# Optimization experiments

Measured on AMD Instinct MI355X. Metric: run time of the kernel, lower is better.

Reference implementation:

```python
import jax, jax.numpy as jnp
import numpy as np
from jax import lax

NBITS = 8
QMAX_SYM = 2 ** (NBITS - 1) - 1  # 127
QMIN_SYM = -(2 ** (NBITS - 1))   # -128
QMAX_ASYM = 2 ** NBITS - 1       # 255


def fake_quant_sym(x):
    # symmetric per-tensor fake quant with straight-through estimator
    delta = lax.stop_gradient(jnp.max(jnp.abs(x))) / QMAX_SYM + 1e-8
    q = jnp.clip(jnp.round(x / delta), QMIN_SYM, QMAX_SYM) * delta
    return x + lax.stop_gradient(q - x)


def fake_quant_asym(x):
    # asymmetric per-tensor fake quant (for softmax output) with STE
    xmin = lax.stop_gradient(jnp.min(x))
    xmax = lax.stop_gradient(jnp.max(x))
    delta = (xmax - xmin) / QMAX_ASYM + 1e-8
    zp = jnp.round(-xmin / delta)
    q = (jnp.clip(jnp.round(x / delta) + zp, 0, QMAX_ASYM) - zp) * delta
    return x + lax.stop_gradient(q - x)


def layer_norm(x, g, b, eps=1e-5):
    mu = jnp.mean(x, axis=-1, keepdims=True)
    var = jnp.var(x, axis=-1, keepdims=True)
    return (x - mu) * lax.rsqrt(var + eps) * g + b


def setup_inputs() -> dict:
    key = jax.random.key(0)
    ks = jax.random.split(key, 8)
    B, N, C = 8, 4096, 256
    s = 0.02
    return {
        "x": jax.random.normal(ks[0], (B, N, C), jnp.float32),
        "q_w": jax.random.normal(ks[1], (C, C), jnp.float32) * s,
        "q_b": jnp.zeros((C,), jnp.float32),
        "kv_w": jax.random.normal(ks[2], (2 * C, C), jnp.float32) * s,
        "kv_b": jnp.zeros((2 * C,), jnp.float32),
        "sr_w": jax.random.normal(ks[3], (C, C, 4, 4), jnp.float32) * s,
        "sr_b": jnp.zeros((C,), jnp.float32),
        "norm_g": jnp.ones((C,), jnp.float32),
        "norm_b": jnp.zeros((C,), jnp.float32),
        "proj_w": jax.random.normal(ks[4], (C, C), jnp.float32) * s,
        "proj_b": jnp.zeros((C,), jnp.float32),
        "H": 64,
        "W": 64,
    }


def reference(x, q_w, q_b, kv_w, kv_b, sr_w, sr_b, norm_g, norm_b, proj_w, proj_b, H, W):
    B, N, C = x.shape
    num_heads = 8
    sr_ratio = 4
    dh = C // num_heads
    scale = dh ** -0.5

    # weight fake-quant (PreQuantModule, sym=True)
    q_wq = fake_quant_sym(q_w)
    kv_wq = fake_quant_sym(kv_w)
    sr_wq = fake_quant_sym(sr_w)
    proj_wq = fake_quant_sym(proj_w)

    # q projection -> [B, heads, N, dh], post-act sym fake quant
    q = (jnp.einsum('bnc,dc->bnd', x, q_wq) + q_b)
    q = fake_quant_sym(q.reshape(B, N, num_heads, dh).transpose(0, 2, 1, 3))

    # spatial reduction: x -> [B,C,H,W], conv k=stride=sr_ratio, then LayerNorm
    x_ = x.transpose(0, 2, 1).reshape(B, C, H, W)
    x_ = lax.conv_general_dilated(x_, sr_wq, (sr_ratio, sr_ratio), 'VALID',
                                  dimension_numbers=('NCHW', 'OIHW', 'NCHW'))
    x_ = x_ + sr_b[None, :, None, None]
    N2 = (H // sr_ratio) * (W // sr_ratio)
    x_ = x_.reshape(B, C, N2).transpose(0, 2, 1)  # [B, N2, C]
    x_ = layer_norm(x_, norm_g, norm_b)

    # kv projection -> k, v [B, heads, N2, dh], post-act sym fake quant
    kv = jnp.einsum('bnc,dc->bnd', x_, kv_wq) + kv_b
    kv = kv.reshape(B, N2, 2, num_heads, dh).transpose(2, 0, 3, 1, 4)
    k = fake_quant_sym(kv[0])
    v = fake_quant_sym(kv[1])

    # attention with asym fake quant on softmax output
    attn = jnp.einsum('bhnd,bhmd->bhnm', q, k) * scale
    attn = jax.nn.softmax(attn, axis=-1)
    attn = fake_quant_asym(attn)

    out = jnp.einsum('bhnm,bhmd->bhnd', attn, v)
    out = out.transpose(0, 2, 1, 3).reshape(B, N, C)
    out = jnp.einsum('bnc,dc->bnd', out, proj_wq) + proj_b
    return out
```

## Files before the change

kernel.cpp:

```cpp
#include <hip/hip_runtime.h>
#include <stdint.h>

typedef float f32x4 __attribute__((ext_vector_type(4)));
typedef __bf16 bf16x8 __attribute__((ext_vector_type(8)));

#define DEV __device__ __forceinline__

DEV unsigned short f2bf(float f) {
  unsigned u = __float_as_uint(f);
  u += 0x7FFFu + ((u >> 16) & 1u);
  return (unsigned short)(u >> 16);
}

DEV float exp2_(float x) {
#if __has_builtin(__builtin_amdgcn_exp2f)
  return __builtin_amdgcn_exp2f(x);
#else
  return exp2f(x);
#endif
}

DEV unsigned cvtpk(float lo, float hi) {
  unsigned r;
  asm("v_cvt_pk_bf16_f32 %0, %1, %2" : "=v"(r) : "v"(lo), "v"(hi));
  return r;
}

DEV void pl32swap(unsigned &a, unsigned &b) {
#if __has_builtin(__builtin_amdgcn_permlane32_swap)
  auto r = __builtin_amdgcn_permlane32_swap(a, b, false, false);
  a = r[0]; b = r[1];
#else
  asm("v_permlane32_swap_b32 %0, %1" : "+v"(a), "+v"(b));
#endif
}

DEV void pl16swap(unsigned &a, unsigned &b) {
#if __has_builtin(__builtin_amdgcn_permlane16_swap)
  auto r = __builtin_amdgcn_permlane16_swap(a, b, false, false);
  a = r[0]; b = r[1];
#else
  asm("v_permlane16_swap_b32 %0, %1" : "+v"(a), "+v"(b));
#endif
}

__global__ void k_init(float* scal) {
  int t = threadIdx.x;
  if (t < 16) scal[t] = (t == 7) ? __uint_as_float(0x7f800000u) : 0.f;
}

__global__ __launch_bounds__(256) void k_absmax4(const float* w0, const float* w1,
                                                 const float* w2, const float* w3, float* scal) {
  const float* srcs[4] = {w0, w1, w2, w3};
  const int ns[4] = {65536, 131072, 1048576, 65536};
  int t = blockIdx.y;
  const float* src = srcs[t];
  int n = ns[t];
  float m = 0.f;
  for (int i = blockIdx.x * 256 + threadIdx.x; i < n; i += gridDim.x * 256)
    m = fmaxf(m, fabsf(src[i]));
  #pragma unroll
  for (int d = 1; d < 64; d <<= 1) m = fmaxf(m, __shfl_xor(m, d, 64));
  __shared__ float red[4];
  if ((threadIdx.x & 63) == 0) red[threadIdx.x >> 6] = m;
  __syncthreads();
  if (threadIdx.x == 0) {
    m = fmaxf(fmaxf(red[0], red[1]), fmaxf(red[2], red[3]));
    atomicMax((unsigned*)(scal + t), __float_as_uint(m));
  }
}

__global__ __launch_bounds__(256) void k_quantw(const float* qw, const float* kvw,
                                                const float* prw, const float* srw,
                                                const float* xf,
                                                unsigned short* qo, unsigned short* kvo,
                                                unsigned short* pro, unsigned short* sro,
                                                unsigned short* xbo,
                                                const float* scal) {
  int bx = blockIdx.x;
  int tid = bx * 256 + threadIdx.x;
  {
    int oo = tid >> 12;
    int rem = tid & 4095;
    int khkw = rem >> 8;
    int i = rem & 255;
    float delta = scal[2] / 127.f + 1e-8f;
    float x = srw[oo * 4096 + i * 16 + khkw];
    sro[tid] = f2bf(fminf(fmaxf(rintf(x / delta), -128.f), 127.f) * delta);
  }
  {
    const float4* xs = (const float4*)(xf + (size_t)tid * 8);
    float4 v0 = xs[0], v1 = xs[1];
    unsigned w0 = ((unsigned)f2bf(v0.y) << 16) | f2bf(v0.x);
    unsigned w1 = ((unsigned)f2bf(v0.w) << 16) | f2bf(v0.z);
    unsigned w2 = ((unsigned)f2bf(v1.y) << 16) | f2bf(v1.x);
    unsigned w3 = ((unsigned)f2bf(v1.w) << 16) | f2bf(v1.z);
    *(uint4*)(xbo + (size_t)tid * 8) = make_uint4(w0, w1, w2, w3);
  }
  if (bx < 512) {
    float delta = scal[1] / 127.f + 1e-8f;
    kvo[tid] = f2bf(fminf(fmaxf(rintf(kvw[tid] / delta), -128.f), 127.f) * delta);
  }
  if (bx < 256) {
    float dq = scal[0] / 127.f + 1e-8f;
    qo[tid] = f2bf(fminf(fmaxf(rintf(qw[tid] / dq), -128.f), 127.f) * dq);
    float dp = scal[3] / 127.f + 1e-8f;
    pro[tid] = f2bf(fminf(fmaxf(rintf(prw[tid] / dp), -128.f), 127.f) * dp);
  }
}

__global__ __launch_bounds__(256) void k_gemm_bk(const unsigned short* __restrict__ Ab,
                                                 const unsigned short* __restrict__ W,
                                                 const float* __restrict__ bias,
                                                 float* __restrict__ C,
                                                 int M, int N, float* max_ptr, int split) {
  __shared__ unsigned short As[64 * 136];
  __shared__ unsigned short Bs[64 * 136];
  const int m0 = blockIdx.y * 64, n0 = blockIdx.x * 64;
  const int tid = threadIdx.x;
  const int wid = tid >> 6, lane = tid & 63;
  const int quad = lane >> 4, lr = lane & 15;
  const int wm = wid >> 1, wn = wid & 1;
  f32x4 acc[2][2] = {};
  for (int kb = 0; kb < 256; kb += 128) {
    __syncthreads();
    #pragma unroll
    for (int i = 0; i < 4; i++) {
      int c = i * 256 + tid;
      int row = c >> 4, cu = (c & 15) * 8;
      *(uint4*)&As[row * 136 + cu] = *(const uint4*)(Ab + (size_t)(m0 + row) * 256 + kb + cu);
      *(uint4*)&Bs[row * 136 + cu] = *(const uint4*)(W + (size_t)(n0 + row) * 256 + kb + cu);
    }
    __syncthreads();
    #pragma unroll
    for (int kc = 0; kc < 4; kc++) {
      bf16x8 af0 = *(const bf16x8*)&As[(wm * 32 + lr) * 136 + kc * 32 + quad * 8];
      bf16x8 af1 = *(const bf16x8*)&As[(wm * 32 + 16 + lr) * 136 + kc * 32 + quad * 8];
      bf16x8 bf0 = *(const bf16x8*)&Bs[(wn * 32 + lr) * 136 + kc * 32 + quad * 8];
      bf16x8 bf1 = *(const bf16x8*)&Bs[(wn * 32 + 16 + lr) * 136 + kc * 32 + quad * 8];
      acc[0][0] = __builtin_amdgcn_mfma_f32_16x16x32_bf16(af0, bf0, acc[0][0], 0, 0, 0);
      acc[0][1] = __builtin_amdgcn_mfma_f32_16x16x32_bf16(af0, bf1, acc[0][1], 0, 0, 0);
      acc[1][0] = __builtin_amdgcn_mfma_f32_16x16x32_bf16(af1, bf0, acc[1][0], 0, 0, 0);
      acc[1][1] = __builtin_amdgcn_mfma_f32_16x16x32_bf16(af1, bf1, acc[1][1], 0, 0, 0);
    }
  }
  float amax = 0.f;
  #pragma unroll
  for (int mi = 0; mi < 2; mi++)
    #pragma unroll
    for (int ni = 0; ni < 2; ni++) {
      int col = n0 + wn * 32 + ni * 16 + lr;
      float bv = bias[col];
      #pragma unroll
      for (int r = 0; r < 4; r++) {
        int row = m0 + wm * 32 + mi * 16 + quad * 4 + r;
        float v = acc[mi][ni][r] + bv;
        C[(size_t)row * N + col] = v;
        amax = fmaxf(amax, fabsf(v));
      }
    }
  if (max_ptr) {
    #pragma unroll
    for (int d = 1; d < 64; d <<= 1) amax = fmaxf(amax, __shfl_xor(amax, d, 64));
    if (lane == 0) {
      int slot = (split > 0 && n0 >= split) ? 1 : 0;
      atomicMax((unsigned*)(max_ptr + slot), __float_as_uint(amax));
    }
  }
}

__global__ __launch_bounds__(256) void k_gemm128(const unsigned short* __restrict__ Ab,
                                                 const unsigned short* __restrict__ W,
                                                 const float* __restrict__ bias,
                                                 float* __restrict__ C,
                                                 float* max_ptr) {
  __shared__ unsigned short As[128 * 72];
  __shared__ unsigned short Bs[128 * 72];
  const int id = blockIdx.x;
  const int xcd = id & 7, idx = id >> 3;
  const int mt = xcd * 32 + (idx >> 1), nt = idx & 1;
  const int m0 = mt * 128, n0 = nt * 128;
  const int tid = threadIdx.x;
  const int wid = tid >> 6, lane = tid & 63;
  const int quad = lane >> 4, lr = lane & 15;
  const int wm = wid >> 1, wn = wid & 1;
  f32x4 acc[4][4] = {};
  for (int kb = 0; kb < 256; kb += 64) {
    __syncthreads();
    #pragma unroll
    for (int i = 0; i < 4; i++) {
      int c = i * 256 + tid;
      int row = c >> 3, cu = (c & 7) * 8;
      *(uint4*)&As[row * 72 + cu] = *(const uint4*)(Ab + (size_t)(m0 + row) * 256 + kb + cu);
      *(uint4*)&Bs[row * 72 + cu] = *(const uint4*)(W + (size_t)(n0 + row) * 256 + kb + cu);
    }
    __syncthreads();
    #pragma unroll
    for (int kc = 0; kc < 2; kc++) {
      bf16x8 af[4], bf[4];
      #pragma unroll
      for (int mi = 0; mi < 4; mi++)
        af[mi] = *(const bf16x8*)&As[(wm * 64 + mi * 16 + lr) * 72 + kc * 32 + quad * 8];
      #pragma unroll
      for (int ni = 0; ni < 4; ni++)
        bf[ni] = *(const bf16x8*)&Bs[(wn * 64 + ni * 16 + lr) * 72 + kc * 32 + quad * 8];
      #pragma unroll
      for (int mi = 0; mi < 4; mi++)
        #pragma unroll
        for (int ni = 0; ni < 4; ni++)
          acc[mi][ni] = __builtin_amdgcn_mfma_f32_16x16x32_bf16(af[mi], bf[ni], acc[mi][ni], 0, 0, 0);
    }
  }
  float amax = 0.f;
  #pragma unroll
  for (int mi = 0; mi < 4; mi++)
    #pragma unroll
    for (int ni = 0; ni < 4; ni++) {
      int col = n0 + wn * 64 + ni * 16 + lr;
      float bv = bias[col];
      #pragma unroll
      for (int r = 0; r < 4; r++) {
        int row = m0 + wm * 64 + mi * 16 + quad * 4 + r;
        float v = acc[mi][ni][r] + bv;
        C[(size_t)row * 256 + col] = v;
        amax = fmaxf(amax, fabsf(v));
      }
    }
  if (max_ptr) {
    #pragma unroll
    for (int d = 1; d < 64; d <<= 1) amax = fmaxf(amax, __shfl_xor(amax, d, 64));
    if (lane == 0) atomicMax((unsigned*)max_ptr, __float_as_uint(amax));
  }
}

__global__ __launch_bounds__(256) void k_conv_sk(const unsigned short* __restrict__ xb,
                                                 const unsigned short* __restrict__ W,
                                                 float* __restrict__ C) {
  __shared__ unsigned short As[64 * 136];
  __shared__ unsigned short Bs[64 * 136];
  const int id = blockIdx.x;
  const int xcd = id & 7, idx = id >> 3;
  const int a = idx >> 2, nt = idx & 3;
  const int ag = xcd * 16 + a;
  const int mt = ag & 31, z = ag >> 5;
  const int m0 = mt * 64, n0 = nt * 64;
  const int kOff = z * 1024;
  C += (size_t)z * 2048 * 256;
  const int tid = threadIdx.x;
  const int wid = tid >> 6, lane = tid & 63;
  const int quad = lane >> 4, lr = lane & 15;
  const int wm = wid >> 1, wn = wid & 1;
  f32x4 acc[2][2] = {};
  for (int kb = 0; kb < 1024; kb += 128) {
    __syncthreads();
    #pragma unroll
    for (int i = 0; i < 4; i++) {
      int c = i * 256 + tid;
      int row = c >> 4, cu = (c & 15) * 8;
      int kk = kOff + kb + cu;
      int m = m0 + row;
      int b = m >> 8, p = m & 255, ph = p >> 4, pw = p & 15;
      int q = kk >> 8, ii = kk & 255;
      int n = (ph * 4 + (q >> 2)) * 64 + pw * 4 + (q & 3);
      *(uint4*)&As[row * 136 + cu] = *(const uint4*)(xb + ((size_t)(b * 4096 + n) * 256 + ii));
      *(uint4*)&Bs[row * 136 + cu] = *(const uint4*)(W + (size_t)(n0 + row) * 4096 + kk);
    }
    __syncthreads();
    #pragma unroll
    for (int kc = 0; kc < 4; kc++) {
      bf16x8 af0 = *(const bf16x8*)&As[(wm * 32 + lr) * 136 + kc * 32 + quad * 8];
      bf16x8 af1 = *(const bf16x8*)&As[(wm * 32 + 16 + lr) * 136 + kc * 32 + quad * 8];
      bf16x8 bf0 = *(const bf16x8*)&Bs[(wn * 32 + lr) * 136 + kc * 32 + quad * 8];
      bf16x8 bf1 = *(const bf16x8*)&Bs[(wn * 32 + 16 + lr) * 136 + kc * 32 + quad * 8];
      acc[0][0] = __builtin_amdgcn_mfma_f32_16x16x32_bf16(af0, bf0, acc[0][0], 0, 0, 0);
      acc[0][1] = __builtin_amdgcn_mfma_f32_16x16x32_bf16(af0, bf1, acc[0][1], 0, 0, 0);
      acc[1][0] = __builtin_amdgcn_mfma_f32_16x16x32_bf16(af1, bf0, acc[1][0], 0, 0, 0);
      acc[1][1] = __builtin_amdgcn_mfma_f32_16x16x32_bf16(af1, bf1, acc[1][1], 0, 0, 0);
    }
  }
  #pragma unroll
  for (int mi = 0; mi < 2; mi++)
    #pragma unroll
    for (int ni = 0; ni < 2; ni++) {
      int col = n0 + wn * 32 + ni * 16 + lr;
      #pragma unroll
      for (int r = 0; r < 4; r++) {
        int row = m0 + wm * 32 + mi * 16 + quad * 4 + r;
        C[(size_t)row * 256 + col] = acc[mi][ni][r];
      }
    }
}

__global__ __launch_bounds__(256) void k_ln(const float* __restrict__ convp, const float* srb,
                                            const float* g, const float* bb,
                                            unsigned short* __restrict__ xn) {
  int row = blockIdx.x, c = threadIdx.x;
  float v = srb[c];
  #pragma unroll
  for (int s = 0; s < 4; s++) v += convp[s * 524288 + row * 256 + c];
  __shared__ float red[4];
  float s = v;
  #pragma unroll
  for (int d = 1; d < 64; d <<= 1) s += __shfl_xor(s, d, 64);
  if ((c & 63) == 0) red[c >> 6] = s;
  __syncthreads();
  float mu = (red[0] + red[1] + red[2] + red[3]) * (1.f / 256.f);
  __syncthreads();
  float dv = v - mu;
  float s2 = dv * dv;
  #pragma unroll
  for (int d = 1; d < 64; d <<= 1) s2 += __shfl_xor(s2, d, 64);
  if ((c & 63) == 0) red[c >> 6] = s2;
  __syncthreads();
  float var = (red[0] + red[1] + red[2] + red[3]) * (1.f / 256.f);
  float rs = 1.f / sqrtf(var + 1e-5f);
  xn[row * 256 + c] = f2bf(dv * rs * g[c] + bb[c]);
}

__global__ __launch_bounds__(256) void k_quant_act(const float* __restrict__ q,
                                                   const float* __restrict__ kv,
                                                   unsigned short* __restrict__ qq,
                                                   unsigned short* __restrict__ kq,
                                                   unsigned short* __restrict__ vqt,
                                                   const float* scal) {
  int bx = blockIdx.x;
  if (bx < 8192) {
    int tid = bx * 256 + threadIdx.x;
    int i4 = tid * 4;
    float delta = scal[4] / 127.f + 1e-8f;
    float4 v = *(const float4*)(q + i4);
    int c = i4 & 255, bn = i4 >> 8;
    int b = bn >> 12, n = bn & 4095;
    int h = c >> 5, j = c & 31;
    ushort4 r;
    r.x = f2bf(fminf(fmaxf(rintf(v.x / delta), -128.f), 127.f) * delta);
    r.y = f2bf(fminf(fmaxf(rintf(v.y / delta), -128.f), 127.f) * delta);
    r.z = f2bf(fminf(fmaxf(rintf(v.z / delta), -128.f), 127.f) * delta);
    r.w = f2bf(fminf(fmaxf(rintf(v.w / delta), -128.f), 127.f) * delta);
    *(ushort4*)(qq + (((size_t)(b * 8 + h) * 4096 + n) * 32) + j) = r;
  } else {
    int tid4 = (bx - 8192) * 256 + threadIdx.x;
    int i4 = tid4 * 4;
    int row = i4 >> 9, d0 = i4 & 511;
    int b = row >> 8, n2 = row & 255;
    int t = d0 >> 8, hj = d0 & 255;
    int h = hj >> 5, j = hj & 31;
    float delta = scal[5 + t] / 127.f + 1e-8f;
    float4 v = *(const float4*)(kv + i4);
    unsigned short r0 = f2bf(fminf(fmaxf(rintf(v.x / delta), -128.f), 127.f) * delta);
    unsigned short r1 = f2bf(fminf(fmaxf(rintf(v.y / delta), -128.f), 127.f) * delta);
    unsigned short r2 = f2bf(fminf(fmaxf(rintf(v.z / delta), -128.f), 127.f) * delta);
    unsigned short r3 = f2bf(fminf(fmaxf(rintf(v.w / delta), -128.f), 127.f) * delta);
    if (t == 0) {
      ushort4 rr = make_ushort4(r0, r1, r2, r3);
      *(ushort4*)(kq + ((size_t)((b * 8 + h) * 256 + n2) * 32) + j) = rr;
    } else {
      size_t base = (size_t)(b * 8 + h) * 32 * 256 + n2;
      vqt[base + (size_t)(j + 0) * 256] = r0;
      vqt[base + (size_t)(j + 1) * 256] = r1;
      vqt[base + (size_t)(j + 2) * 256] = r2;
      vqt[base + (size_t)(j + 3) * 256] = r3;
    }
  }
}

__global__ __launch_bounds__(256) void k_attn1(const unsigned short* __restrict__ qq,
                                               const unsigned short* __restrict__ kq,
                                               float2* __restrict__ rowstats,
                                               float2* __restrict__ pstat) {
  __shared__ unsigned short KsL[8192];
  __shared__ float red[8];
  const int bh = blockIdx.y;
  const int row0 = blockIdx.x * 256;
  const int tid = threadIdx.x, wid = tid >> 6, lane = tid & 63, quad = lane >> 4, lr = lane & 15;
  const float c2 = 0.17677669529663687f * 1.4426950408889634f;
  const unsigned short* kb = kq + (size_t)bh * 8192;
  #pragma unroll
  for (int k = 0; k < 4; k++) {
    int cid = k * 256 + tid;
    int seg = cid >> 6, lc = cid & 63, qc = lc >> 4, lrc = lc & 15;
    *(uint4*)&KsL[cid * 8] = *(const uint4*)(kb + (seg * 16 + lrc) * 32 + qc * 8);
  }
  __syncthreads();
  float wmin = 1e30f, wmax = 0.f;
  #pragma unroll
  for (int g = 0; g < 4; g++) {
    int rowg = row0 + g * 64 + wid * 16 + lr;
    bf16x8 qf = *(const bf16x8*)(qq + ((size_t)bh * 4096 + rowg) * 32 + quad * 8);
    f32x4 acc[16] = {};
    #pragma unroll
    for (int t = 0; t < 16; t++) {
      bf16x8 kf = *(const bf16x8*)&KsL[(t * 64 + quad * 16 + lr) * 8];
      acc[t] = __builtin_amdgcn_mfma_f32_16x16x32_bf16(kf, qf, acc[t], 0, 0, 0);
    }
    float mxr = -1e30f, mnr = 1e30f;
    #pragma unroll
    for (int t = 0; t < 16; t++)
      #pragma unroll
      for (int r = 0; r < 4; r++) {
        float s = acc[t][r];
        mxr = fmaxf(mxr, s); mnr = fminf(mnr, s);
      }
    #pragma unroll
    for (int d = 16; d < 64; d <<= 1) {
      mxr = fmaxf(mxr, __shfl_xor(mxr, d, 64));
      mnr = fminf(mnr, __shfl_xor(mnr, d, 64));
    }
    float m2 = mxr * c2;
    float l = 0.f;
    #pragma unroll
    for (int t = 0; t < 16; t++)
      #pragma unroll
      for (int r = 0; r < 4; r++)
        l += exp2_(fmaf(acc[t][r], c2, -m2));
    #pragma unroll
    for (int d = 16; d < 64; d <<= 1) l += __shfl_xor(l, d, 64);
    float inv_l = 1.f / l;
    if (lane < 16)
      rowstats[(size_t)bh * 4096 + rowg] = make_float2(m2, inv_l);
    wmax = fmaxf(wmax, inv_l);
    wmin = fminf(wmin, exp2_((mnr - mxr) * c2) * inv_l);
  }
  #pragma unroll
  for (int d = 1; d < 16; d <<= 1) {
    wmax = fmaxf(wmax, __shfl_xor(wmax, d, 64));
    wmin = fminf(wmin, __shfl_xor(wmin, d, 64));
  }
  if (lane == 0) { red[wid] = wmin; red[4 + wid] = wmax; }
  __syncthreads();
  if (tid == 0) {
    float mn = fminf(fminf(red[0], red[1]), fminf(red[2], red[3]));
    float mx = fmaxf(fmaxf(red[4], red[5]), fmaxf(red[6], red[7]));
    pstat[blockIdx.y * 16 + blockIdx.x] = make_float2(mn, mx);
  }
}

__global__ __launch_bounds__(256) void k_pminmax(const float2* __restrict__ pstat, float* scal) {
  int t = threadIdx.x;
  float mn = 1e30f, mx = 0.f;
  #pragma unroll
  for (int i = 0; i < 4; i++) {
    float2 v = pstat[t + i * 256];
    mn = fminf(mn, v.x); mx = fmaxf(mx, v.y);
  }
  #pragma unroll
  for (int d = 1; d < 64; d <<= 1) {
    mn = fminf(mn, __shfl_xor(mn, d, 64));
    mx = fmaxf(mx, __shfl_xor(mx, d, 64));
  }
  __shared__ float red[8];
  if ((t & 63) == 0) { red[t >> 6] = mn; red[4 + (t >> 6)] = mx; }
  __syncthreads();
  if (t == 0) {
    scal[7] = fminf(fminf(red[0], red[1]), fminf(red[2], red[3]));
    scal[8] = fmaxf(fmaxf(red[4], red[5]), fmaxf(red[6], red[7]));
  }
}

__global__ __launch_bounds__(256) void k_attn2(const unsigned short* __restrict__ qq,
                                               const unsigned short* __restrict__ kq,
                                               const unsigned short* __restrict__ vqt,
                                               const float* scal,
                                               const float2* __restrict__ rowstats,
                                               unsigned short* __restrict__ attn_out) {
  __shared__ unsigned short KsL[8192];
  __shared__ unsigned short VsL[8192];
  const int bh = blockIdx.y, b = bh >> 3, h = bh & 7;
  const int row0 = blockIdx.x * 256;
  const int tid = threadIdx.x, wid = tid >> 6, lane = tid & 63, quad = lane >> 4, lr = lane & 15;
  const float c2 = 0.17677669529663687f * 1.4426950408889634f;
  const unsigned short* kb = kq + (size_t)bh * 8192;
  const unsigned short* vb = vqt + (size_t)bh * 8192;
  #pragma unroll
  for (int k = 0; k < 4; k++) {
    int cid = k * 256 + tid;
    int seg = cid >> 6, lc = cid & 63, qc = lc >> 4, lrc = lc & 15;
    *(uint4*)&KsL[cid * 8] = *(const uint4*)(kb + (seg * 16 + lrc) * 32 + qc * 8);
    *(uint4*)&VsL[cid * 8] =
        *(const uint4*)(vb + ((seg & 1) * 16 + lrc) * 256 + (seg >> 1) * 32 + qc * 8);
  }
  float pmin = scal[7], pmax = scal[8];
  float delta = (pmax - pmin) / 255.f + 1e-8f;
  float zp = rintf(-pmin / delta);
  float qlo = -zp, qhi = 255.f - zp;
  __syncthreads();
  #pragma unroll
  for (int g = 0; g < 4; g++) {
    int rowg = row0 + g * 64 + wid * 16 + lr;
    bf16x8 qf = *(const bf16x8*)(qq + ((size_t)bh * 4096 + rowg) * 32 + quad * 8);
    float2 st = rowstats[(size_t)bh * 4096 + rowg];
    f32x4 acc[16] = {};
    #pragma unroll
    for (int t = 0; t < 16; t++) {
      bf16x8 kf = *(const bf16x8*)&KsL[(t * 64 + quad * 16 + lr) * 8];
      acc[t] = __builtin_amdgcn_mfma_f32_16x16x32_bf16(kf, qf, acc[t], 0, 0, 0);
    }
    float ofs = __log2f(st.y / delta) - st.x;
    f32x4 o0 = {}, o1 = {};
    #pragma unroll
    for (int ks = 0; ks < 8; ks++) {
      float pv[8];
      #pragma unroll
      for (int half = 0; half < 2; half++) {
        #pragma unroll
        for (int r = 0; r < 4; r++) {
          float v = exp2_(fmaf(acc[2 * ks + half][r], c2, ofs));
          pv[half * 4 + r] = fminf(fmaxf(rintf(v), qlo), qhi) * delta;
        }
      }
      unsigned wa = cvtpk(pv[0], pv[1]);
      unsigned wb = cvtpk(pv[2], pv[3]);
      unsigned wc = cvtpk(pv[4], pv[5]);
      unsigned wd = cvtpk(pv[6], pv[7]);
      pl32swap(wa, wc);
      pl16swap(wa, wc);
      pl32swap(wb, wd);
      pl16swap(wb, wd);
      uint4 w = make_uint4(wa, wb, wc, wd);
      bf16x8 pa = *(bf16x8*)&w;
      bf16x8 b0 = *(const bf16x8*)&VsL[((ks * 2 + 0) * 64 + quad * 16 + lr) * 8];
      bf16x8 b1 = *(const bf16x8*)&VsL[((ks * 2 + 1) * 64 + quad * 16 + lr) * 8];
      o0 = __builtin_amdgcn_mfma_f32_16x16x32_bf16(pa, b0, o0, 0, 0, 0);
      o1 = __builtin_amdgcn_mfma_f32_16x16x32_bf16(pa, b1, o1, 0, 0, 0);
    }
    #pragma unroll
    for (int r = 0; r < 4; r++) {
      int n = row0 + g * 64 + wid * 16 + quad * 4 + r;
      size_t base = ((size_t)(b * 4096) + n) * 256 + h * 32;
      attn_out[base + lr] = f2bf(o0[r]);
      attn_out[base + 16 + lr] = f2bf(o1[r]);
    }
  }
}

extern "C" void kernel_launch(void* const* d_in, const int* in_sizes, int n_in,
                              void* d_out, int out_size, void* d_ws, size_t ws_size,
                              hipStream_t stream) {
  const float* x      = (const float*)d_in[0];
  const float* q_w    = (const float*)d_in[1];
  const float* q_b    = (const float*)d_in[2];
  const float* kv_w   = (const float*)d_in[3];
  const float* kv_b   = (const float*)d_in[4];
  const float* sr_w   = (const float*)d_in[5];
  const float* sr_b   = (const float*)d_in[6];
  const float* norm_g = (const float*)d_in[7];
  const float* norm_b = (const float*)d_in[8];
  const float* proj_w = (const float*)d_in[9];
  const float* proj_b = (const float*)d_in[10];
  float* out = (float*)d_out;

  char* ws = (char*)d_ws;
  float* scal = (float*)ws;
  unsigned short* q_wq    = (unsigned short*)(ws + 256);
  unsigned short* kv_wq   = (unsigned short*)(ws + 131328);
  unsigned short* proj_wq = (unsigned short*)(ws + 393472);
  unsigned short* sr_wq   = (unsigned short*)(ws + 524544);
  unsigned short* xn      = (unsigned short*)(ws + 2621696);
  float*          kv_f    = (float*)(ws + 3670272);
  unsigned short* kq      = (unsigned short*)(ws + 7864576);
  unsigned short* vqt     = (unsigned short*)(ws + 8913152);
  float2*         rowstats= (float2*)(ws + 9961728);
  float*          convp   = (float*)(ws + 12058880);
  float*          q_f     = (float*)(ws + 12058880);
  unsigned short* qq      = (unsigned short*)(ws + 45613312);
  unsigned short* xb      = (unsigned short*)(ws + 62390528);
  unsigned short* attn_o  = (unsigned short*)(ws + 12058880);
  float2*         pstat   = (float2*)(ws + 28836096);

  k_init<<<1, 64, 0, stream>>>(scal);
  k_absmax4<<<dim3(64, 4), 256, 0, stream>>>(q_w, kv_w, sr_w, proj_w, scal);
  k_quantw<<<4096, 256, 0, stream>>>(q_w, kv_w, proj_w, sr_w, x,
                                     q_wq, kv_wq, proj_wq, sr_wq, xb, scal);
  k_conv_sk<<<512, 256, 0, stream>>>(xb, sr_wq, convp);
  k_ln<<<2048, 256, 0, stream>>>(convp, sr_b, norm_g, norm_b, xn);
  k_gemm_bk<<<dim3(8, 32), 256, 0, stream>>>(xn, kv_wq, kv_b, kv_f, 2048, 512, scal + 5, 256);
  k_gemm128<<<512, 256, 0, stream>>>(xb, q_wq, q_b, q_f, scal + 4);
  k_quant_act<<<9216, 256, 0, stream>>>(q_f, kv_f, qq, kq, vqt, scal);
  k_attn1<<<dim3(16, 64), 256, 0, stream>>>(qq, kq, rowstats, pstat);
  k_pminmax<<<1, 256, 0, stream>>>(pstat, scal);
  k_attn2<<<dim3(16, 64), 256, 0, stream>>>(qq, kq, vqt, scal, rowstats, attn_o);
  k_gemm128<<<512, 256, 0, stream>>>(attn_o, proj_wq, proj_b, out, nullptr);
}
```

Baseline: 272.2 us.

## Fuse q fake-quant into attention loads and drop separate min/max kernel

The q projection GEMM now writes bf16 directly in head-major layout instead of an fp32 buffer. Both attention kernels re-apply the symmetric fake quant to q fragments as they load them. This removes the fp32 q round trip through memory and the q half of the activation-quant kernel. Separately, the per-block softmax min/max is merged with atomics into the scalar slots, which removes the single-block reduction kernel. The cost is that q is quantized from a bf16-rounded value rather than fp32, which can move rounding at quant-bin boundaries, and the dequant work is repeated in both attention passes.

```diff
diff --git a/kernel.cpp b/kernel.cpp
--- a/kernel.cpp
+++ b/kernel.cpp
@@ -42,6 +42,21 @@
 #else
   asm("v_permlane16_swap_b32 %0, %1" : "+v"(a), "+v"(b));
 #endif
+}
+
+DEV bf16x8 qfrag(uint4 w, float idq, float dq) {
+  unsigned o[4];
+  const unsigned* wi = &w.x;
+  #pragma unroll
+  for (int i = 0; i < 4; i++) {
+    float lo = __uint_as_float(wi[i] << 16);
+    float hi = __uint_as_float(wi[i] & 0xffff0000u);
+    lo = fminf(fmaxf(rintf(lo * idq), -128.f), 127.f) * dq;
+    hi = fminf(fmaxf(rintf(hi * idq), -128.f), 127.f) * dq;
+    o[i] = cvtpk(lo, hi);
+  }
+  uint4 r = make_uint4(o[0], o[1], o[2], o[3]);
+  return *(bf16x8*)&r;
 }
 
 __global__ void k_init(float* scal) {
@@ -169,10 +184,11 @@
   }
 }
 
+template<int MODE>
 __global__ __launch_bounds__(256) void k_gemm128(const unsigned short* __restrict__ Ab,
                                                  const unsigned short* __restrict__ W,
                                                  const float* __restrict__ bias,
-                                                 float* __restrict__ C,
+                                                 void* __restrict__ Cout,
                                                  float* max_ptr) {
   __shared__ unsigned short As[128 * 72];
   __shared__ unsigned short Bs[128 * 72];
@@ -222,7 +238,13 @@
       for (int r = 0; r < 4; r++) {
         int row = m0 + wm * 64 + mi * 16 + quad * 4 + r;
         float v = acc[mi][ni][r] + bv;
-        C[(size_t)row * 256 + col] = v;
+        if (MODE == 0) {
+          ((float*)Cout)[(size_t)row * 256 + col] = v;
+        } else {
+          int b = row >> 12, nn = row & 4095;
+          int h = col >> 5, j = col & 31;
+          ((unsigned short*)Cout)[((size_t)(b * 8 + h) * 4096 + nn) * 32 + j] = f2bf(v);
+        }
         amax = fmaxf(amax, fabsf(v));
       }
     }
@@ -317,57 +339,38 @@
   xn[row * 256 + c] = f2bf(dv * rs * g[c] + bb[c]);
 }
 
-__global__ __launch_bounds__(256) void k_quant_act(const float* __restrict__ q,
-                                                   const float* __restrict__ kv,
-                                                   unsigned short* __restrict__ qq,
-                                                   unsigned short* __restrict__ kq,
-                                                   unsigned short* __restrict__ vqt,
-                                                   const float* scal) {
-  int bx = blockIdx.x;
-  if (bx < 8192) {
-    int tid = bx * 256 + threadIdx.x;
-    int i4 = tid * 4;
-    float delta = scal[4] / 127.f + 1e-8f;
-    float4 v = *(const float4*)(q + i4);
-    int c = i4 & 255, bn = i4 >> 8;
-    int b = bn >> 12, n = bn & 4095;
-    int h = c >> 5, j = c & 31;
-    ushort4 r;
-    r.x = f2bf(fminf(fmaxf(rintf(v.x / delta), -128.f), 127.f) * delta);
-    r.y = f2bf(fminf(fmaxf(rintf(v.y / delta), -128.f), 127.f) * delta);
-    r.z = f2bf(fminf(fmaxf(rintf(v.z / delta), -128.f), 127.f) * delta);
-    r.w = f2bf(fminf(fmaxf(rintf(v.w / delta), -128.f), 127.f) * delta);
-    *(ushort4*)(qq + (((size_t)(b * 8 + h) * 4096 + n) * 32) + j) = r;
+__global__ __launch_bounds__(256) void k_quant_kv(const float* __restrict__ kv,
+                                                  unsigned short* __restrict__ kq,
+                                                  unsigned short* __restrict__ vqt,
+                                                  const float* scal) {
+  int tid4 = blockIdx.x * 256 + threadIdx.x;
+  int i4 = tid4 * 4;
+  int row = i4 >> 9, d0 = i4 & 511;
+  int b = row >> 8, n2 = row & 255;
+  int t = d0 >> 8, hj = d0 & 255;
+  int h = hj >> 5, j = hj & 31;
+  float delta = scal[5 + t] / 127.f + 1e-8f;
+  float4 v = *(const float4*)(kv + i4);
+  unsigned short r0 = f2bf(fminf(fmaxf(rintf(v.x / delta), -128.f), 127.f) * delta);
+  unsigned short r1 = f2bf(fminf(fmaxf(rintf(v.y / delta), -128.f), 127.f) * delta);
+  unsigned short r2 = f2bf(fminf(fmaxf(rintf(v.z / delta), -128.f), 127.f) * delta);
+  unsigned short r3 = f2bf(fminf(fmaxf(rintf(v.w / delta), -128.f), 127.f) * delta);
+  if (t == 0) {
+    ushort4 rr = make_ushort4(r0, r1, r2, r3);
+    *(ushort4*)(kq + ((size_t)((b * 8 + h) * 256 + n2) * 32) + j) = rr;
   } else {
-    int tid4 = (bx - 8192) * 256 + threadIdx.x;
-    int i4 = tid4 * 4;
-    int row = i4 >> 9, d0 = i4 & 511;
-    int b = row >> 8, n2 = row & 255;
-    int t = d0 >> 8, hj = d0 & 255;
-    int h = hj >> 5, j = hj & 31;
-    float delta = scal[5 + t] / 127.f + 1e-8f;
-    float4 v = *(const float4*)(kv + i4);
-    unsigned short r0 = f2bf(fminf(fmaxf(rintf(v.x / delta), -128.f), 127.f) * delta);
-    unsigned short r1 = f2bf(fminf(fmaxf(rintf(v.y / delta), -128.f), 127.f) * delta);
-    unsigned short r2 = f2bf(fminf(fmaxf(rintf(v.z / delta), -128.f), 127.f) * delta);
-    unsigned short r3 = f2bf(fminf(fmaxf(rintf(v.w / delta), -128.f), 127.f) * delta);
-    if (t == 0) {
-      ushort4 rr = make_ushort4(r0, r1, r2, r3);
-      *(ushort4*)(kq + ((size_t)((b * 8 + h) * 256 + n2) * 32) + j) = rr;
-    } else {
-      size_t base = (size_t)(b * 8 + h) * 32 * 256 + n2;
-      vqt[base + (size_t)(j + 0) * 256] = r0;
-      vqt[base + (size_t)(j + 1) * 256] = r1;
-      vqt[base + (size_t)(j + 2) * 256] = r2;
-      vqt[base + (size_t)(j + 3) * 256] = r3;
-    }
+    size_t base = (size_t)(b * 8 + h) * 32 * 256 + n2;
+    vqt[base + (size_t)(j + 0) * 256] = r0;
+    vqt[base + (size_t)(j + 1) * 256] = r1;
+    vqt[base + (size_t)(j + 2) * 256] = r2;
+    vqt[base + (size_t)(j + 3) * 256] = r3;
   }
 }
 
 __global__ __launch_bounds__(256) void k_attn1(const unsigned short* __restrict__ qq,
                                                const unsigned short* __restrict__ kq,
                                                float2* __restrict__ rowstats,
-                                               float2* __restrict__ pstat) {
+                                               float* scal) {
   __shared__ unsigned short KsL[8192];
   __shared__ float red[8];
   const int bh = blockIdx.y;
@@ -381,12 +384,15 @@
     int seg = cid >> 6, lc = cid & 63, qc = lc >> 4, lrc = lc & 15;
     *(uint4*)&KsL[cid * 8] = *(const uint4*)(kb + (seg * 16 + lrc) * 32 + qc * 8);
   }
+  float dq = scal[4] / 127.f + 1e-8f;
+  float idq = 1.f / dq;
   __syncthreads();
   float wmin = 1e30f, wmax = 0.f;
   #pragma unroll
   for (int g = 0; g < 4; g++) {
     int rowg = row0 + g * 64 + wid * 16 + lr;
-    bf16x8 qf = *(const bf16x8*)(qq + ((size_t)bh * 4096 + rowg) * 32 + quad * 8);
+    uint4 qw = *(const uint4*)(qq + ((size_t)bh * 4096 + rowg) * 32 + quad * 8);
+    bf16x8 qf = qfrag(qw, idq, dq);
     f32x4 acc[16] = {};
     #pragma unroll
     for (int t = 0; t < 16; t++) {
@@ -431,29 +437,8 @@
   if (tid == 0) {
     float mn = fminf(fminf(red[0], red[1]), fminf(red[2], red[3]));
     float mx = fmaxf(fmaxf(red[4], red[5]), fmaxf(red[6], red[7]));
-    pstat[blockIdx.y * 16 + blockIdx.x] = make_float2(mn, mx);
-  }
-}
-
-__global__ __launch_bounds__(256) void k_pminmax(const float2* __restrict__ pstat, float* scal) {
-  int t = threadIdx.x;
-  float mn = 1e30f, mx = 0.f;
-  #pragma unroll
-  for (int i = 0; i < 4; i++) {
-    float2 v = pstat[t + i * 256];
-    mn = fminf(mn, v.x); mx = fmaxf(mx, v.y);
-  }
-  #pragma unroll
-  for (int d = 1; d < 64; d <<= 1) {
-    mn = fminf(mn, __shfl_xor(mn, d, 64));
-    mx = fmaxf(mx, __shfl_xor(mx, d, 64));
-  }
-  __shared__ float red[8];
-  if ((t & 63) == 0) { red[t >> 6] = mn; red[4 + (t >> 6)] = mx; }
-  __syncthreads();
-  if (t == 0) {
-    scal[7] = fminf(fminf(red[0], red[1]), fminf(red[2], red[3]));
-    scal[8] = fmaxf(fmaxf(red[4], red[5]), fmaxf(red[6], red[7]));
+    atomicMin((unsigned*)(scal + 7), __float_as_uint(mn));
+    atomicMax((unsigned*)(scal + 8), __float_as_uint(mx));
   }
 }
 
@@ -479,6 +464,8 @@
     *(uint4*)&VsL[cid * 8] =
         *(const uint4*)(vb + ((seg & 1) * 16 + lrc) * 256 + (seg >> 1) * 32 + qc * 8);
   }
+  float dq = scal[4] / 127.f + 1e-8f;
+  float idq = 1.f / dq;
   float pmin = scal[7], pmax = scal[8];
   float delta = (pmax - pmin) / 255.f + 1e-8f;
   float zp = rintf(-pmin / delta);
@@ -487,7 +474,8 @@
   #pragma unroll
   for (int g = 0; g < 4; g++) {
     int rowg = row0 + g * 64 + wid * 16 + lr;
-    bf16x8 qf = *(const bf16x8*)(qq + ((size_t)bh * 4096 + rowg) * 32 + quad * 8);
+    uint4 qw = *(const uint4*)(qq + ((size_t)bh * 4096 + rowg) * 32 + quad * 8);
+    bf16x8 qf = qfrag(qw, idq, dq);
     float2 st = rowstats[(size_t)bh * 4096 + rowg];
     f32x4 acc[16] = {};
     #pragma unroll
@@ -561,11 +549,9 @@
   unsigned short* vqt     = (unsigned short*)(ws + 8913152);
   float2*         rowstats= (float2*)(ws + 9961728);
   float*          convp   = (float*)(ws + 12058880);
-  float*          q_f     = (float*)(ws + 12058880);
+  unsigned short* attn_o  = (unsigned short*)(ws + 12058880);
   unsigned short* qq      = (unsigned short*)(ws + 45613312);
   unsigned short* xb      = (unsigned short*)(ws + 62390528);
-  unsigned short* attn_o  = (unsigned short*)(ws + 12058880);
-  float2*         pstat   = (float2*)(ws + 28836096);
 
   k_init<<<1, 64, 0, stream>>>(scal);
   k_absmax4<<<dim3(64, 4), 256, 0, stream>>>(q_w, kv_w, sr_w, proj_w, scal);
@@ -574,10 +560,9 @@
   k_conv_sk<<<512, 256, 0, stream>>>(xb, sr_wq, convp);
   k_ln<<<2048, 256, 0, stream>>>(convp, sr_b, norm_g, norm_b, xn);
   k_gemm_bk<<<dim3(8, 32), 256, 0, stream>>>(xn, kv_wq, kv_b, kv_f, 2048, 512, scal + 5, 256);
-  k_gemm128<<<512, 256, 0, stream>>>(xb, q_wq, q_b, q_f, scal + 4);
-  k_quant_act<<<9216, 256, 0, stream>>>(q_f, kv_f, qq, kq, vqt, scal);
-  k_attn1<<<dim3(16, 64), 256, 0, stream>>>(qq, kq, rowstats, pstat);
-  k_pminmax<<<1, 256, 0, stream>>>(pstat, scal);
+  k_gemm128<1><<<512, 256, 0, stream>>>(xb, q_wq, q_b, qq, scal + 4);
+  k_quant_kv<<<1024, 256, 0, stream>>>(kv_f, kq, vqt, scal);
+  k_attn1<<<dim3(16, 64), 256, 0, stream>>>(qq, kq, rowstats, scal);
   k_attn2<<<dim3(16, 64), 256, 0, stream>>>(qq, kq, vqt, scal, rowstats, attn_o);
-  k_gemm128<<<512, 256, 0, stream>>>(attn_o, proj_wq, proj_b, out, nullptr);
-}
+  k_gemm128<0><<<512, 256, 0, stream>>>(attn_o, proj_wq, proj_b, out, nullptr);
+}
```

Result: no change. 277.3 us (+1.9%).
